# Kernel tuning notes

Hardware: AMD Instinct MI355X
Metric: run time of the kernel (lower is better)

The kernel has to match this reference:

```python
import jax, jax.numpy as jnp
import numpy as np

B, T, D, K = 16, 4096, 512, 256
ALPHA_MIN = 1e-6


def setup_inputs() -> dict:
    key = jax.random.key(0)
    ks = jax.random.split(key, 5)
    x = jax.random.normal(ks[0], (B, T, D), dtype=jnp.float32)
    # s_imag ~ U(-pi, pi) as in reset_parameters
    s_imag = jax.random.uniform(ks[1], (K,), minval=-np.pi, maxval=np.pi, dtype=jnp.float32)
    # s_real_raw = softplus^{-1}(target_alpha - alpha_min), target_alpha ~ U(0.01, 0.2)
    target_alpha = jax.random.uniform(ks[2], (K,), minval=0.01, maxval=0.2, dtype=jnp.float32)
    y = jnp.clip(target_alpha - ALPHA_MIN, 1e-8, None)
    s_real_raw = jnp.log(jnp.expm1(y))
    # projection weight/bias (spectral norm applied inside reference)
    W = jax.random.normal(ks[3], (K, D), dtype=jnp.float32) / np.sqrt(D)
    b = jnp.zeros((K,), dtype=jnp.float32)
    tau_raw = jnp.zeros((), dtype=jnp.float32)
    return {"x": x, "s_real_raw": s_real_raw, "s_imag": s_imag,
            "tau_raw": tau_raw, "W": W, "b": b}


def _spectral_normalize(W):
    # one power iteration from a fixed random u (mirrors torch spectral_norm buffer,
    # n_power_iterations=1, eps=1e-7); u,v are stop-gradiented like torch buffers.
    eps = 1e-7
    u0 = jax.random.normal(jax.random.key(42), (W.shape[0],), dtype=W.dtype)
    u0 = u0 / jnp.maximum(jnp.linalg.norm(u0), eps)
    v = W.T @ u0
    v = v / jnp.maximum(jnp.linalg.norm(v), eps)
    u = W @ v
    u = u / jnp.maximum(jnp.linalg.norm(u), eps)
    u = jax.lax.stop_gradient(u)
    v = jax.lax.stop_gradient(v)
    sigma = u @ (W @ v)
    return W / sigma


def reference(x, s_real_raw, s_imag, tau_raw, W, b):
    Bx, Tx, Dx = x.shape
    k = s_imag.shape[0]
    tau = jax.nn.softplus(tau_raw) + 1e-3
    alpha0 = (jax.nn.softplus(s_real_raw) + ALPHA_MIN) * tau  # [k]
    omega0 = s_imag * tau                                     # [k]
    # dt is None path: uniform normalized time step
    dt = jnp.asarray(1.0 / max(Tx - 1, 1), dtype=x.dtype)
    rho = jnp.exp(-alpha0 * dt)   # [k], time-invariant since dt is constant
    ct = jnp.cos(omega0 * dt)     # [k]
    st = jnp.sin(omega0 * dt)     # [k]
    # spectral-normalized linear drive u_t = W_sn x_t + b  -> [B,T,k]
    u = jnp.einsum('btd,kd->btk', x, _spectral_normalize(W)) + b

    def step(carry, u_t):
        c, s = carry  # each [B,k]
        c_new = rho * (c * ct - s * st) + u_t
        s_new = rho * (c * st + s * ct)
        return (c_new, s_new), (c_new, s_new)

    z0 = (jnp.zeros((Bx, k), x.dtype), jnp.zeros((Bx, k), x.dtype))
    _, (C, S) = jax.lax.scan(step, z0, jnp.swapaxes(u, 0, 1))  # [T,B,k] each
    C = jnp.swapaxes(C, 0, 1)
    S = jnp.swapaxes(S, 0, 1)
    return jnp.concatenate([C, S], axis=2)  # [B,T,2k]
```

## Files before the change

### kernel.cpp

```cpp
#include <hip/hip_runtime.h>

#define Bsz 16
#define Tsz 4096
#define Dsz 512
#define Ksz 256
#define Msz (Bsz * Tsz)
#define CHUNK 64
#define NCH (Tsz / CHUNK)

typedef __attribute__((ext_vector_type(8))) short short8;
typedef __attribute__((ext_vector_type(4))) float f32x4;

__device__ __forceinline__ unsigned int rotl32(unsigned int x, int d) {
  return (x << d) | (x >> (32 - d));
}

__device__ void threefry_pair(unsigned int c0, unsigned int c1,
                              unsigned int& o0, unsigned int& o1) {
  const unsigned int k0 = 0u, k1 = 42u;
  const unsigned int k2 = k0 ^ k1 ^ 0x1BD11BDAu;
  unsigned int x0 = c0 + k0;
  unsigned int x1 = c1 + k1;
#define TF_ROUND(r) { x0 += x1; x1 = rotl32(x1, (r)); x1 ^= x0; }
  TF_ROUND(13) TF_ROUND(15) TF_ROUND(26) TF_ROUND(6)
  x0 += k1; x1 += k2 + 1u;
  TF_ROUND(17) TF_ROUND(29) TF_ROUND(16) TF_ROUND(24)
  x0 += k2; x1 += k0 + 2u;
  TF_ROUND(13) TF_ROUND(15) TF_ROUND(26) TF_ROUND(6)
  x0 += k0; x1 += k1 + 3u;
  TF_ROUND(17) TF_ROUND(29) TF_ROUND(16) TF_ROUND(24)
  x0 += k1; x1 += k2 + 4u;
  TF_ROUND(13) TF_ROUND(15) TF_ROUND(26) TF_ROUND(6)
  x0 += k2; x1 += k0 + 5u;
#undef TF_ROUND
  o0 = x0; o1 = x1;
}

__device__ float erfinv32(float x) {
  float w = -log1pf(-x * x);
  float p;
  if (w < 5.f) {
    w -= 2.5f;
    p = 2.81022636e-08f;
    p = fmaf(p, w, 3.43273939e-07f);
    p = fmaf(p, w, -3.5233877e-06f);
    p = fmaf(p, w, -4.39150654e-06f);
    p = fmaf(p, w, 0.00021858087f);
    p = fmaf(p, w, -0.00125372503f);
    p = fmaf(p, w, -0.00417768164f);
    p = fmaf(p, w, 0.246640727f);
    p = fmaf(p, w, 1.50140941f);
  } else {
    w = sqrtf(w) - 3.f;
    p = -0.000200214257f;
    p = fmaf(p, w, 0.000100950558f);
    p = fmaf(p, w, 0.00134934322f);
    p = fmaf(p, w, -0.00367342844f);
    p = fmaf(p, w, 0.00573950773f);
    p = fmaf(p, w, -0.0076224613f);
    p = fmaf(p, w, 0.00943887047f);
    p = fmaf(p, w, 1.00167406f);
    p = fmaf(p, w, 2.83297682f);
  }
  return p * x;
}

__device__ float bits_to_normal(unsigned int bits) {
  unsigned int fb = (bits >> 9) | 0x3f800000u;
  float f = __uint_as_float(fb) - 1.0f;
  const float lo = -0.99999994f;
  float u = f * 2.0f + lo;
  u = fmaxf(lo, u);
  return 1.41421356f * erfinv32(u);
}

__device__ float block_sum_512(float v, float* s_red) {
  #pragma unroll
  for (int o = 32; o > 0; o >>= 1) v += __shfl_down(v, o);
  const int lane = threadIdx.x & 63, wid = threadIdx.x >> 6;
  if (lane == 0) s_red[wid] = v;
  __syncthreads();
  float r = 0.f;
  #pragma unroll
  for (int i = 0; i < 8; ++i) r += s_red[i];
  __syncthreads();
  return r;
}

__device__ __forceinline__ unsigned int bf16rne(float f) {
  unsigned int u = __float_as_uint(f);
  return (u + 0x7FFFu + ((u >> 16) & 1u)) >> 16;
}

__global__ __launch_bounds__(512) void prep1_kernel(
    const float* __restrict__ W, float* __restrict__ partial_v) {
  __shared__ float s_u0[Ksz];
  __shared__ float s_red[8];
  const int tid = threadIdx.x;
  if (tid < 128) {
    unsigned int y0, y1;
    threefry_pair((unsigned int)tid, (unsigned int)(tid + 128), y0, y1);
    s_u0[tid] = bits_to_normal(y0);
    s_u0[tid + 128] = bits_to_normal(y1);
  }
  __syncthreads();
  float val = (tid < Ksz) ? s_u0[tid] * s_u0[tid] : 0.f;
  float ss = block_sum_512(val, s_red);
  float inv = 1.f / fmaxf(sqrtf(ss), 1e-7f);

  const int k0 = blockIdx.x * 16;
  float acc = 0.f;
  #pragma unroll
  for (int kk = 0; kk < 16; ++kk)
    acc = fmaf(W[(size_t)(k0 + kk) * Dsz + tid], s_u0[k0 + kk], acc);
  partial_v[blockIdx.x * Dsz + tid] = acc * inv;
}

__global__ __launch_bounds__(512) void prep2_kernel(
    const float* __restrict__ W, const float* __restrict__ partial_v,
    float* __restrict__ wv) {
  __shared__ float s_v[Dsz];
  __shared__ float s_red[8];
  __shared__ float s_p[8];
  const int tid = threadIdx.x;
  float acc = 0.f;
  #pragma unroll
  for (int b = 0; b < 16; ++b) acc += partial_v[b * Dsz + tid];
  float ssv = block_sum_512(acc * acc, s_red);
  float invv = 1.f / fmaxf(sqrtf(ssv), 1e-7f);
  s_v[tid] = acc * invv;
  __syncthreads();

  const int k = blockIdx.x * 4 + (tid >> 7);
  const int sub = tid & 127;
  const float* wr = W + (size_t)k * Dsz;
  float p = 0.f;
  #pragma unroll
  for (int j = sub; j < Dsz; j += 128) p = fmaf(wr[j], s_v[j], p);
  #pragma unroll
  for (int o = 32; o > 0; o >>= 1) p += __shfl_down(p, o);
  const int lane = tid & 63, wid = tid >> 6;
  if (lane == 0) s_p[wid] = p;
  __syncthreads();
  if (tid < 4) wv[blockIdx.x * 4 + tid] = s_p[2 * tid] + s_p[2 * tid + 1];
}

__global__ __launch_bounds__(256) void prep3_kernel(
    const float* __restrict__ s_real_raw, const float* __restrict__ s_imag,
    const float* __restrict__ tau_raw, const float* __restrict__ wv,
    float* __restrict__ consts) {
  __shared__ float s_p[4];
  const int tid = threadIdx.x;
  float v = wv[tid];
  float v2 = v * v;
  #pragma unroll
  for (int o = 32; o > 0; o >>= 1) v2 += __shfl_down(v2, o);
  const int lane = tid & 63, wid = tid >> 6;
  if (lane == 0) s_p[wid] = v2;
  __syncthreads();
  float sswv = s_p[0] + s_p[1] + s_p[2] + s_p[3];
  float sigma = sswv / fmaxf(sqrtf(sswv), 1e-7f);
  if (tid == 0) consts[10 * Ksz] = 1.f / sigma;

  float tr = tau_raw[0];
  float tau = fmaxf(tr, 0.f) + log1pf(expf(-fabsf(tr))) + 1e-3f;
  float srr = s_real_raw[tid];
  float sp = fmaxf(srr, 0.f) + log1pf(expf(-fabsf(srr)));
  float alpha0 = (sp + 1e-6f) * tau;
  float omega0 = s_imag[tid] * tau;
  const float dt = 1.f / 4095.f;
  float ad = alpha0 * dt, an = omega0 * dt;
  consts[tid]            = expf(-ad) * cosf(an);
  consts[Ksz + tid]      = expf(-ad) * sinf(an);
  consts[2 * Ksz + tid]  = expf(-ad * 64.f) * cosf(an * 64.f);
  consts[3 * Ksz + tid]  = expf(-ad * 64.f) * sinf(an * 64.f);
  consts[4 * Ksz + tid]  = expf(-ad * 4.f) * cosf(an * 4.f);
  consts[5 * Ksz + tid]  = expf(-ad * 4.f) * sinf(an * 4.f);
  consts[6 * Ksz + tid]  = expf(-ad * 8.f) * cosf(an * 8.f);
  consts[7 * Ksz + tid]  = expf(-ad * 8.f) * sinf(an * 8.f);
  consts[8 * Ksz + tid]  = expf(-ad * 16.f) * cosf(an * 16.f);
  consts[9 * Ksz + tid]  = expf(-ad * 16.f) * sinf(an * 16.f);
}

__global__ __launch_bounds__(64) void wpack_kernel(
    const float* __restrict__ W, const float* __restrict__ consts,
    unsigned int* __restrict__ WfH, unsigned int* __restrict__ WfL) {
  const int kb = blockIdx.x >> 4;
  const int nb = blockIdx.x & 15;
  const int lane = threadIdx.x;
  const int lr = lane & 15, lg = lane >> 4;
  const float inv_sigma = consts[10 * Ksz];
  const float* src = W + (size_t)(nb * 16 + lr) * Dsz + kb * 32 + lg * 8;
  float v[8];
  *(float4*)&v[0] = *(const float4*)src;
  *(float4*)&v[4] = *(const float4*)(src + 4);
  unsigned int hh[4], ll[4];
  #pragma unroll
  for (int i = 0; i < 4; ++i) {
    float v0 = v[2 * i] * inv_sigma, v1 = v[2 * i + 1] * inv_sigma;
    unsigned int u0 = __float_as_uint(v0);
    unsigned int u1 = __float_as_uint(v1);
    hh[i] = (u0 >> 16) | (u1 & 0xFFFF0000u);
    float r0 = v0 - __uint_as_float(u0 & 0xFFFF0000u);
    float r1 = v1 - __uint_as_float(u1 & 0xFFFF0000u);
    ll[i] = bf16rne(r0) | (bf16rne(r1) << 16);
  }
  const size_t off = (size_t)blockIdx.x * 256 + lane * 4;
  *(int4*)(WfH + off) = *(int4*)hh;
  *(int4*)(WfL + off) = *(int4*)ll;
}

__global__ __launch_bounds__(256, 2) void gemm_mfma(
    const float* __restrict__ X, const unsigned int* __restrict__ WfH,
    const unsigned int* __restrict__ WfL, const float* __restrict__ bias,
    const float* __restrict__ consts, float* __restrict__ U,
    float* __restrict__ carry) {
  __shared__ unsigned int ldsA[2][2048];

  const int tid = threadIdx.x;
  const size_t m0 = (size_t)blockIdx.x * 64;

  const int sr = tid >> 2;
  const int sc = (tid & 3) * 8;
  const float* gx = X + (m0 + sr) * Dsz + sc;
  const int swz = (sr & 7) << 4;
  const int aoff_h = sr * 128 + ((sc * 2) ^ swz);
  const int aoff_l = sr * 128 + ((64 + sc * 2) ^ swz);

  const int lane = tid & 63;
  const int wn = tid >> 6;
  const int lr = lane & 15;
  const int lg = lane >> 4;

  float xaA[8], xaB[8];
  #define LOAD_A(dst, kb) do {                             \
    const float* p = gx + (kb) * 32;                       \
    *(float4*)&dst[0] = *(const float4*)p;                 \
    *(float4*)&dst[4] = *(const float4*)(p + 4);           \
  } while (0)

  const char* const wfh = (const char*)WfH + (size_t)wn * 4096 + lane * 16;
  const char* const wfl = (const char*)WfL + (size_t)wn * 4096 + lane * 16;

  short8 bhA[4], blA[4], bhB[4], blB[4];
  #define LOAD_B(bh_, bl_, kb) do {                                          \
    const size_t tb = (size_t)(kb) * 16384;                                  \
    _Pragma("unroll")                                                        \
    for (int f = 0; f < 4; ++f) {                                            \
      bh_[f] = *(const short8*)(wfh + tb + (size_t)f * 1024);                \
      bl_[f] = *(const short8*)(wfl + tb + (size_t)f * 1024);                \
    }                                                                        \
  } while (0)

  #define CONVERT_STORE(xa, buf) do {                                        \
    char* const Ab_ = (char*)ldsA[(buf)];                                    \
    unsigned int hh[4], llw[4];                                              \
    _Pragma("unroll")                                                        \
    for (int i = 0; i < 4; ++i) {                                            \
      float v0 = xa[2 * i], v1 = xa[2 * i + 1];                              \
      unsigned int u0 = __float_as_uint(v0);                                 \
      unsigned int u1 = __float_as_uint(v1);                                 \
      hh[i] = (u0 >> 16) | (u1 & 0xFFFF0000u);                               \
      float r0 = v0 - __uint_as_float(u0 & 0xFFFF0000u);                     \
      float r1 = v1 - __uint_as_float(u1 & 0xFFFF0000u);                     \
      llw[i] = bf16rne(r0) | (bf16rne(r1) << 16);                            \
    }                                                                        \
    *(int4*)(Ab_ + aoff_h) = *(int4*)hh;                                     \
    *(int4*)(Ab_ + aoff_l) = *(int4*)llw;                                    \
  } while (0)

  #define DS_READ(ah_, al_, buf) do {                                        \
    const char* const Ab_ = (const char*)ldsA[(buf)];                        \
    _Pragma("unroll")                                                        \
    for (int f = 0; f < 4; ++f) {                                            \
      const int r = f * 16 + lr;                                             \
      const int sz = (r & 7) << 4;                                           \
      ah_[f] = *(const short8*)(Ab_ + r * 128 + ((lg * 16) ^ sz));           \
      al_[f] = *(const short8*)(Ab_ + r * 128 + ((64 + lg * 16) ^ sz));      \
    }                                                                        \
  } while (0)

  #define MFMA48(ah_, al_, bh_, bl_) do {                                    \
    _Pragma("unroll")                                                        \
    for (int mf = 0; mf < 4; ++mf)                                           \
      _Pragma("unroll")                                                      \
      for (int nf = 0; nf < 4; ++nf)                                         \
        acc[mf][nf] = __builtin_amdgcn_mfma_f32_16x16x32_bf16(               \
            ah_[mf], bh_[nf], acc[mf][nf], 0, 0, 0);                         \
    _Pragma("unroll")                                                        \
    for (int mf = 0; mf < 4; ++mf)                                           \
      _Pragma("unroll")                                                      \
      for (int nf = 0; nf < 4; ++nf)                                         \
        acc[mf][nf] = __builtin_amdgcn_mfma_f32_16x16x32_bf16(               \
            ah_[mf], bl_[nf], acc[mf][nf], 0, 0, 0);                         \
    _Pragma("unroll")                                                        \
    for (int mf = 0; mf < 4; ++mf)                                           \
      _Pragma("unroll")                                                      \
      for (int nf = 0; nf < 4; ++nf)                                         \
        acc[mf][nf] = __builtin_amdgcn_mfma_f32_16x16x32_bf16(               \
            al_[mf], bh_[nf], acc[mf][nf], 0, 0, 0);                         \
  } while (0)

  #define SYNC() do {                                                        \
    asm volatile("s_waitcnt lgkmcnt(0)" ::: "memory");                       \
    __builtin_amdgcn_s_barrier();                                            \
    __builtin_amdgcn_sched_barrier(0);                                       \
  } while (0)

  f32x4 acc[4][4];
  #pragma unroll
  for (int i = 0; i < 4; ++i)
    #pragma unroll
    for (int j = 0; j < 4; ++j) acc[i][j] = (f32x4)(0.f);

  short8 ahA[4], alA[4], ahB[4], alB[4];

  LOAD_A(xaA, 0);
  LOAD_A(xaB, 1);
  LOAD_B(bhA, blA, 0);
  CONVERT_STORE(xaA, 0);
  LOAD_A(xaA, 2);
  SYNC();
  DS_READ(ahA, alA, 0);
  CONVERT_STORE(xaB, 1);
  LOAD_A(xaB, 3);
  SYNC();

  #define BODY(kb, fragCh, fragCl, fragNh, fragNl, bCh, bCl, bNh, bNl, xa)   \
  do {                                                                       \
    if ((kb) + 1 < 16) DS_READ(fragNh, fragNl, ((kb) + 1) & 1);              \
    MFMA48(fragCh, fragCl, bCh, bCl);                                        \
    if ((kb) + 2 < 16) CONVERT_STORE(xa, (kb) & 1);            \
    if ((kb) + 4 < 16) LOAD_A(xa, (kb) + 4);                                 \
    if ((kb) + 1 < 16) LOAD_B(bNh, bNl, (kb) + 1);                           \
    SYNC();                                                                  \
  } while (0)

  for (int kb = 0; kb < 16; kb += 2) {
    BODY(kb,     ahA, alA, ahB, alB, bhA, blA, bhB, blB, xaA);
    BODY(kb + 1, ahB, alB, ahA, alA, bhB, blB, bhA, blA, xaB);
  }
  #undef BODY
  #undef SYNC
  #undef MFMA48
  #undef DS_READ
  #undef CONVERT_STORE
  #undef LOAD_B
  #undef LOAD_A

  #pragma unroll
  for (int nf = 0; nf < 4; ++nf) {
    const int n = wn * 64 + nf * 16 + lr;
    const float bv = bias[n];
    const float ar_ = consts[n],           ai_ = consts[Ksz + n];
    const float p4r = consts[4 * Ksz + n], p4i = consts[5 * Ksz + n];
    const float p8r = consts[6 * Ksz + n], p8i = consts[7 * Ksz + n];
    const float p16r = consts[8 * Ksz + n], p16i = consts[9 * Ksz + n];
    const int e = 3 - lg;
    const float b1r = (e & 1) ? p4r : 1.f, b1i = (e & 1) ? p4i : 0.f;
    const float b2r = (e & 2) ? p8r : 1.f, b2i = (e & 2) ? p8i : 0.f;
    float wr = b1r * b2r - b1i * b2i;
    float wi = b1r * b2i + b1i * b2r;
    float Sr = 0.f, Si = 0.f;
    #pragma unroll
    for (int mf = 3; mf >= 0; --mf) {
      float vr = wr, vi = wi;
      #pragma unroll
      for (int j = 3; j >= 0; --j) {
        const float u = acc[mf][nf][j] + bv;
        U[(m0 + mf * 16 + lg * 4 + j) * Ksz + n] = u;
        Sr = fmaf(u, vr, Sr);
        Si = fmaf(u, vi, Si);
        if (j) {
          float t_ = vr * ar_ - vi * ai_;
          vi = vr * ai_ + vi * ar_;
          vr = t_;
        }
      }
      if (mf) {
        float t_ = wr * p16r - wi * p16i;
        wi = wr * p16i + wi * p16r;
        wr = t_;
      }
    }
    Sr += __shfl_xor(Sr, 16); Si += __shfl_xor(Si, 16);
    Sr += __shfl_xor(Sr, 32); Si += __shfl_xor(Si, 32);
    if (lg == 0)
      ((float2*)carry)[(size_t)blockIdx.x * Ksz + n] = make_float2(Sr, Si);
  }
}

__global__ __launch_bounds__(64) void scan_prefix(
    const float* __restrict__ consts, const float* __restrict__ carry,
    float* __restrict__ prefix) {
  const int k = blockIdx.y * 64 + threadIdx.x;
  const int b = blockIdx.x;
  const float Ar = consts[2 * Ksz + k], Ai = consts[3 * Ksz + k];
  const float2* cp = (const float2*)carry;
  float2* pp = (float2*)prefix;
  float c = 0.f, s = 0.f;
  for (int m = 0; m < NCH; ++m) {
    const size_t idx = (size_t)(b * NCH + m) * Ksz + k;
    pp[idx] = make_float2(c, s);
    float2 L = cp[idx];
    float cn = fmaf(Ar, c, fmaf(-Ai, s, L.x));
    float sn = fmaf(Ai, c, fmaf(Ar, s, L.y));
    c = cn; s = sn;
  }
}

__global__ __launch_bounds__(256) void scan_final(
    const float* __restrict__ U, const float* __restrict__ consts,
    const float* __restrict__ prefix, float* __restrict__ out) {
  const int k = threadIdx.x;
  const int bm = blockIdx.x;
  const float ar = consts[k], ai = consts[Ksz + k];
  float2 w = ((const float2*)prefix)[(size_t)bm * Ksz + k];
  float c = w.x, s = w.y;
  const float* up = U + (size_t)bm * (CHUNK * Ksz) + k;
  float* op = out + (size_t)bm * (CHUNK * 2 * Ksz);
  #pragma unroll 4
  for (int t = 0; t < CHUNK; ++t) {
    float u = up[(size_t)t * Ksz];
    float cn = fmaf(ar, c, fmaf(-ai, s, u));
    s = fmaf(ai, c, ar * s);
    c = cn;
    op[(size_t)t * 2 * Ksz + k] = c;
    op[(size_t)t * 2 * Ksz + Ksz + k] = s;
  }
}

extern "C" void kernel_launch(void* const* d_in, const int* in_sizes, int n_in,
                              void* d_out, int out_size, void* d_ws, size_t ws_size,
                              hipStream_t stream) {
  const float* x    = (const float*)d_in[0];
  const float* srr  = (const float*)d_in[1];
  const float* sim  = (const float*)d_in[2];
  const float* traw = (const float*)d_in[3];
  const float* W    = (const float*)d_in[4];
  const float* bias = (const float*)d_in[5];
  float* out = (float*)d_out;

  float* wsf    = (float*)d_ws;
  float* consts = wsf;
  float* U      = wsf + 4096;
  float* carry  = U + (size_t)Msz * Ksz;
  float* prefix = carry + (size_t)2 * Bsz * NCH * Ksz;
  unsigned int* WfH = (unsigned int*)(prefix + (size_t)2 * Bsz * NCH * Ksz);
  unsigned int* WfL = WfH + 65536;
  float* partial_v  = (float*)(WfL + 65536);
  float* wv         = partial_v + 16 * Dsz;

  prep1_kernel<<<16, 512, 0, stream>>>(W, partial_v);
  prep2_kernel<<<64, 512, 0, stream>>>(W, partial_v, wv);
  prep3_kernel<<<1, 256, 0, stream>>>(srr, sim, traw, wv, consts);
  wpack_kernel<<<256, 64, 0, stream>>>(W, consts, WfH, WfL);
  gemm_mfma<<<Msz / 64, 256, 0, stream>>>(x, WfH, WfL, bias, consts, U, carry);
  scan_prefix<<<dim3(Bsz, Ksz / 64), 64, 0, stream>>>(consts, carry, prefix);
  scan_final<<<Bsz * NCH, Ksz, 0, stream>>>(U, consts, prefix, out);
}
```

Baseline: 127.2 us.

## Split GEMM tile across 8 waves with two M-halves and LDS carry reduction

The 64-row GEMM block now runs with 512 threads in 8 waves instead of 4, with each wave computing 32 rows by 64 columns instead of 64 by 64. This halves per-wave accumulator and fragment registers, aiming for more resident waves and better latency hiding. The B-operand register double buffering is dropped and B is loaded each step right before its MFMAs, which can expose global-load latency. Per-chunk carry contributions from the two M-halves are combined through LDS, using a new precomputed 32-step decay constant, at the cost of an extra block barrier.

```diff
diff --git a/kernel.cpp b/kernel.cpp
--- a/kernel.cpp
+++ b/kernel.cpp
@@ -160,7 +160,7 @@
   __syncthreads();
   float sswv = s_p[0] + s_p[1] + s_p[2] + s_p[3];
   float sigma = sswv / fmaxf(sqrtf(sswv), 1e-7f);
-  if (tid == 0) consts[10 * Ksz] = 1.f / sigma;
+  if (tid == 0) consts[12 * Ksz] = 1.f / sigma;
 
   float tr = tau_raw[0];
   float tau = fmaxf(tr, 0.f) + log1pf(expf(-fabsf(tr))) + 1e-3f;
@@ -180,6 +180,8 @@
   consts[7 * Ksz + tid]  = expf(-ad * 8.f) * sinf(an * 8.f);
   consts[8 * Ksz + tid]  = expf(-ad * 16.f) * cosf(an * 16.f);
   consts[9 * Ksz + tid]  = expf(-ad * 16.f) * sinf(an * 16.f);
+  consts[10 * Ksz + tid] = expf(-ad * 32.f) * cosf(an * 32.f);
+  consts[11 * Ksz + tid] = expf(-ad * 32.f) * sinf(an * 32.f);
 }
 
 __global__ __launch_bounds__(64) void wpack_kernel(
@@ -189,7 +191,7 @@
   const int nb = blockIdx.x & 15;
   const int lane = threadIdx.x;
   const int lr = lane & 15, lg = lane >> 4;
-  const float inv_sigma = consts[10 * Ksz];
+  const float inv_sigma = consts[12 * Ksz];
   const float* src = W + (size_t)(nb * 16 + lr) * Dsz + kb * 32 + lg * 8;
   float v[8];
   *(float4*)&v[0] = *(const float4*)src;
@@ -210,7 +212,7 @@
   *(int4*)(WfL + off) = *(int4*)ll;
 }
 
-__global__ __launch_bounds__(256, 2) void gemm_mfma(
+__global__ __launch_bounds__(512, 3) void gemm_mfma(
     const float* __restrict__ X, const unsigned int* __restrict__ WfH,
     const unsigned int* __restrict__ WfL, const float* __restrict__ bias,
     const float* __restrict__ consts, float* __restrict__ U,
@@ -220,43 +222,43 @@
   const int tid = threadIdx.x;
   const size_t m0 = (size_t)blockIdx.x * 64;
 
-  const int sr = tid >> 2;
-  const int sc = (tid & 3) * 8;
+  const int sr = tid >> 3;
+  const int sc = (tid & 7) * 4;
   const float* gx = X + (m0 + sr) * Dsz + sc;
   const int swz = (sr & 7) << 4;
   const int aoff_h = sr * 128 + ((sc * 2) ^ swz);
   const int aoff_l = sr * 128 + ((64 + sc * 2) ^ swz);
 
   const int lane = tid & 63;
-  const int wn = tid >> 6;
+  const int wid = tid >> 6;
+  const int wm = wid >> 2;
+  const int wn2 = wid & 3;
   const int lr = lane & 15;
   const int lg = lane >> 4;
 
-  float xaA[8], xaB[8];
-  #define LOAD_A(dst, kb) do {                             \
-    const float* p = gx + (kb) * 32;                       \
-    *(float4*)&dst[0] = *(const float4*)p;                 \
-    *(float4*)&dst[4] = *(const float4*)(p + 4);           \
-  } while (0)
-
-  const char* const wfh = (const char*)WfH + (size_t)wn * 4096 + lane * 16;
-  const char* const wfl = (const char*)WfL + (size_t)wn * 4096 + lane * 16;
-
-  short8 bhA[4], blA[4], bhB[4], blB[4];
-  #define LOAD_B(bh_, bl_, kb) do {                                          \
+  float xaA[4], xaB[4];
+  #define LOAD_A(dst, kb) do {                                               \
+    *(float4*)&dst[0] = *(const float4*)(gx + (kb) * 32);                    \
+  } while (0)
+
+  const char* const wfh = (const char*)WfH + (size_t)wn2 * 4096 + lane * 16;
+  const char* const wfl = (const char*)WfL + (size_t)wn2 * 4096 + lane * 16;
+
+  short8 bh[4], bl[4];
+  #define LOAD_B(kb) do {                                                    \
     const size_t tb = (size_t)(kb) * 16384;                                  \
     _Pragma("unroll")                                                        \
     for (int f = 0; f < 4; ++f) {                                            \
-      bh_[f] = *(const short8*)(wfh + tb + (size_t)f * 1024);                \
-      bl_[f] = *(const short8*)(wfl + tb + (size_t)f * 1024);                \
+      bh[f] = *(const short8*)(wfh + tb + (size_t)f * 1024);                 \
+      bl[f] = *(const short8*)(wfl + tb + (size_t)f * 1024);                 \
     }                                                                        \
   } while (0)
 
   #define CONVERT_STORE(xa, buf) do {                                        \
     char* const Ab_ = (char*)ldsA[(buf)];                                    \
-    unsigned int hh[4], llw[4];                                              \
-    _Pragma("unroll")                                                        \
-    for (int i = 0; i < 4; ++i) {                                            \
+    unsigned int hh[2], llw[2];                                              \
+    _Pragma("unroll")                                                        \
+    for (int i = 0; i < 2; ++i) {                                            \
       float v0 = xa[2 * i], v1 = xa[2 * i + 1];                              \
       unsigned int u0 = __float_as_uint(v0);                                 \
       unsigned int u1 = __float_as_uint(v1);                                 \
@@ -265,40 +267,47 @@
       float r1 = v1 - __uint_as_float(u1 & 0xFFFF0000u);                     \
       llw[i] = bf16rne(r0) | (bf16rne(r1) << 16);                            \
     }                                                                        \
-    *(int4*)(Ab_ + aoff_h) = *(int4*)hh;                                     \
-    *(int4*)(Ab_ + aoff_l) = *(int4*)llw;                                    \
-  } while (0)
-
-  #define DS_READ(ah_, al_, buf) do {                                        \
+    *(int2*)(Ab_ + aoff_h) = *(int2*)hh;                                     \
+    *(int2*)(Ab_ + aoff_l) = *(int2*)llw;                                    \
+  } while (0)
+
+  short8 ah[2], al[2];
+  #define DS_READ(buf) do {                                                  \
     const char* const Ab_ = (const char*)ldsA[(buf)];                        \
     _Pragma("unroll")                                                        \
-    for (int f = 0; f < 4; ++f) {                                            \
-      const int r = f * 16 + lr;                                             \
+    for (int f = 0; f < 2; ++f) {                                            \
+      const int r = wm * 32 + f * 16 + lr;                                   \
       const int sz = (r & 7) << 4;                                           \
-      ah_[f] = *(const short8*)(Ab_ + r * 128 + ((lg * 16) ^ sz));           \
-      al_[f] = *(const short8*)(Ab_ + r * 128 + ((64 + lg * 16) ^ sz));      \
+      ah[f] = *(const short8*)(Ab_ + r * 128 + ((lg * 16) ^ sz));            \
+      al[f] = *(const short8*)(Ab_ + r * 128 + ((64 + lg * 16) ^ sz));       \
     }                                                                        \
   } while (0)
 
-  #define MFMA48(ah_, al_, bh_, bl_) do {                                    \
-    _Pragma("unroll")                                                        \
-    for (int mf = 0; mf < 4; ++mf)                                           \
+  f32x4 acc[2][4];
+  #pragma unroll
+  for (int i = 0; i < 2; ++i)
+    #pragma unroll
+    for (int j = 0; j < 4; ++j) acc[i][j] = (f32x4)(0.f);
+
+  #define MFMA24() do {                                                      \
+    _Pragma("unroll")                                                        \
+    for (int mf = 0; mf < 2; ++mf)                                           \
       _Pragma("unroll")                                                      \
       for (int nf = 0; nf < 4; ++nf)                                         \
         acc[mf][nf] = __builtin_amdgcn_mfma_f32_16x16x32_bf16(               \
-            ah_[mf], bh_[nf], acc[mf][nf], 0, 0, 0);                         \
-    _Pragma("unroll")                                                        \
-    for (int mf = 0; mf < 4; ++mf)                                           \
+            ah[mf], bh[nf], acc[mf][nf], 0, 0, 0);                           \
+    _Pragma("unroll")                                                        \
+    for (int mf = 0; mf < 2; ++mf)                                           \
       _Pragma("unroll")                                                      \
       for (int nf = 0; nf < 4; ++nf)                                         \
         acc[mf][nf] = __builtin_amdgcn_mfma_f32_16x16x32_bf16(               \
-            ah_[mf], bl_[nf], acc[mf][nf], 0, 0, 0);                         \
-    _Pragma("unroll")                                                        \
-    for (int mf = 0; mf < 4; ++mf)                                           \
+            ah[mf], bl[nf], acc[mf][nf], 0, 0, 0);                           \
+    _Pragma("unroll")                                                        \
+    for (int mf = 0; mf < 2; ++mf)                                           \
       _Pragma("unroll")                                                      \
       for (int nf = 0; nf < 4; ++nf)                                         \
         acc[mf][nf] = __builtin_amdgcn_mfma_f32_16x16x32_bf16(               \
-            al_[mf], bh_[nf], acc[mf][nf], 0, 0, 0);                         \
+            al[mf], bh[nf], acc[mf][nf], 0, 0, 0);                           \
   } while (0)
 
   #define SYNC() do {                                                        \
@@ -307,50 +316,37 @@
     __builtin_amdgcn_sched_barrier(0);                                       \
   } while (0)
 
-  f32x4 acc[4][4];
-  #pragma unroll
-  for (int i = 0; i < 4; ++i)
-    #pragma unroll
-    for (int j = 0; j < 4; ++j) acc[i][j] = (f32x4)(0.f);
-
-  short8 ahA[4], alA[4], ahB[4], alB[4];
-
   LOAD_A(xaA, 0);
   LOAD_A(xaB, 1);
-  LOAD_B(bhA, blA, 0);
   CONVERT_STORE(xaA, 0);
   LOAD_A(xaA, 2);
   SYNC();
-  DS_READ(ahA, alA, 0);
-  CONVERT_STORE(xaB, 1);
-  LOAD_A(xaB, 3);
-  SYNC();
-
-  #define BODY(kb, fragCh, fragCl, fragNh, fragNl, bCh, bCl, bNh, bNl, xa)   \
-  do {                                                                       \
-    if ((kb) + 1 < 16) DS_READ(fragNh, fragNl, ((kb) + 1) & 1);              \
-    MFMA48(fragCh, fragCl, bCh, bCl);                                        \
-    if ((kb) + 2 < 16) CONVERT_STORE(xa, (kb) & 1);            \
-    if ((kb) + 4 < 16) LOAD_A(xa, (kb) + 4);                                 \
-    if ((kb) + 1 < 16) LOAD_B(bNh, bNl, (kb) + 1);                           \
+
+  #define BODY(kb, xa) do {                                                  \
+    DS_READ((kb) & 1);                                \
+    LOAD_B(kb);                                    \
+    if ((kb) + 1 < 16) CONVERT_STORE(xa, ((kb) + 1) & 1);                    \
+    if ((kb) + 3 < 16) LOAD_A(xa, (kb) + 3);                                 \
+    MFMA24();                                                                \
     SYNC();                                                                  \
   } while (0)
 
   for (int kb = 0; kb < 16; kb += 2) {
-    BODY(kb,     ahA, alA, ahB, alB, bhA, blA, bhB, blB, xaA);
-    BODY(kb + 1, ahB, alB, ahA, alA, bhB, blB, bhA, blA, xaB);
+    BODY(kb,     xaB);
+    BODY(kb + 1, xaA);
   }
   #undef BODY
   #undef SYNC
-  #undef MFMA48
+  #undef MFMA24
   #undef DS_READ
   #undef CONVERT_STORE
   #undef LOAD_B
   #undef LOAD_A
 
+  float2* scratch = (float2*)ldsA;
   #pragma unroll
   for (int nf = 0; nf < 4; ++nf) {
-    const int n = wn * 64 + nf * 16 + lr;
+    const int n = wn2 * 64 + nf * 16 + lr;
     const float bv = bias[n];
     const float ar_ = consts[n],           ai_ = consts[Ksz + n];
     const float p4r = consts[4 * Ksz + n], p4i = consts[5 * Ksz + n];
@@ -363,12 +359,12 @@
     float wi = b1r * b2i + b1i * b2r;
     float Sr = 0.f, Si = 0.f;
     #pragma unroll
-    for (int mf = 3; mf >= 0; --mf) {
+    for (int mf = 1; mf >= 0; --mf) {
       float vr = wr, vi = wi;
       #pragma unroll
       for (int j = 3; j >= 0; --j) {
         const float u = acc[mf][nf][j] + bv;
-        U[(m0 + mf * 16 + lg * 4 + j) * Ksz + n] = u;
+        U[(m0 + wm * 32 + mf * 16 + lg * 4 + j) * Ksz + n] = u;
         Sr = fmaf(u, vr, Sr);
         Si = fmaf(u, vi, Si);
         if (j) {
@@ -385,8 +381,25 @@
     }
     Sr += __shfl_xor(Sr, 16); Si += __shfl_xor(Si, 16);
     Sr += __shfl_xor(Sr, 32); Si += __shfl_xor(Si, 32);
-    if (lg == 0)
-      ((float2*)carry)[(size_t)blockIdx.x * Ksz + n] = make_float2(Sr, Si);
+    if (lg == 0) {
+      float pr = Sr, pi = Si;
+      if (wm == 0) {
+        const float p32r = consts[10 * Ksz + n], p32i = consts[11 * Ksz + n];
+        pr = Sr * p32r - Si * p32i;
+        pi = Sr * p32i + Si * p32r;
+      }
+      scratch[wm * 256 + n] = make_float2(pr, pi);
+    }
+  }
+  __syncthreads();
+  if (wm == 0 && lg == 0) {
+    #pragma unroll
+    for (int nf = 0; nf < 4; ++nf) {
+      const int n = wn2 * 64 + nf * 16 + lr;
+      float2 a0 = scratch[n], a1 = scratch[256 + n];
+      ((float2*)carry)[(size_t)blockIdx.x * Ksz + n] =
+          make_float2(a0.x + a1.x, a0.y + a1.y);
+    }
   }
 }
 
@@ -455,7 +468,7 @@
   prep2_kernel<<<64, 512, 0, stream>>>(W, partial_v, wv);
   prep3_kernel<<<1, 256, 0, stream>>>(srr, sim, traw, wv, consts);
   wpack_kernel<<<256, 64, 0, stream>>>(W, consts, WfH, WfL);
-  gemm_mfma<<<Msz / 64, 256, 0, stream>>>(x, WfH, WfL, bias, consts, U, carry);
+  gemm_mfma<<<Msz / 64, 512, 0, stream>>>(x, WfH, WfL, bias, consts, U, carry);
   scan_prefix<<<dim3(Bsz, Ksz / 64), 64, 0, stream>>>(consts, carry, prefix);
   scan_final<<<Bsz * NCH, Ksz, 0, stream>>>(U, consts, prefix, out);
 }
```

Result: slower. 151.2 us (+18.9%).
